# Optimization experiments

Measured on AMD Instinct MI355X. Metric: run time of the kernel, lower is better.

The kernel has to match this reference:

```python
import jax, jax.numpy as jnp
import numpy as np

N_NODES = 100000
N_EDGES = 1600000
IN_CH = 128
OUT_CH = 32
HEADS = 2
NEG_SLOPE = 0.2  # GATv2Conv default negative_slope


def setup_inputs() -> dict:
    key = jax.random.key(0)
    ks = jax.random.split(key, 6)
    x = jax.random.normal(ks[0], (N_NODES, IN_CH), dtype=jnp.float32)
    edge_index = jax.random.randint(ks[1], (2, N_EDGES), 0, N_NODES, dtype=jnp.int64)
    s_in = 1.0 / np.sqrt(IN_CH)
    Wl = jax.random.normal(ks[2], (IN_CH, HEADS * OUT_CH), dtype=jnp.float32) * s_in  # lin_l weight
    Wr = jax.random.normal(ks[3], (IN_CH, HEADS * OUT_CH), dtype=jnp.float32) * s_in  # lin_r weight
    bl = jnp.zeros((HEADS * OUT_CH,), dtype=jnp.float32)
    br = jnp.zeros((HEADS * OUT_CH,), dtype=jnp.float32)
    att = jax.random.normal(ks[4], (HEADS, OUT_CH), dtype=jnp.float32) * (1.0 / np.sqrt(OUT_CH))
    bias = jnp.zeros((OUT_CH,), dtype=jnp.float32)  # output bias (concat=False -> size out_channels)
    return {"x": x, "Wl": Wl, "bl": bl, "Wr": Wr, "br": br, "att": att, "bias": bias,
            "edge_index": edge_index}


def _gatv2_layer(x, Wl, bl, Wr, br, att, bias, edge_index):
    N = x.shape[0]
    H, C = att.shape
    # add self loops (GATv2Conv default add_self_loops=True)
    loops = jnp.arange(N, dtype=edge_index.dtype)
    src = jnp.concatenate([edge_index[0], loops])  # [E+N] message sources j
    dst = jnp.concatenate([edge_index[1], loops])  # [E+N] message targets i
    # per-node linear transforms (share_weights=False)
    xl = (x @ Wl + bl).reshape(N, H, C)
    xr = (x @ Wr + br).reshape(N, H, C)
    # GATv2 dynamic attention: a^T LeakyReLU(xl[j] + xr[i])
    h = xl[src] + xr[dst]                                   # [E, H, C]
    e = jnp.einsum('ehc,hc->eh', jax.nn.leaky_relu(h, NEG_SLOPE), att)  # [E, H]
    # segment softmax over incoming edges of each target node
    m = jax.ops.segment_max(e, dst, num_segments=N)         # [N, H]
    a = jnp.exp(e - m[dst])
    denom = jax.ops.segment_sum(a, dst, num_segments=N)     # [N, H]
    alpha = a / (denom[dst] + 1e-16)                        # [E, H]
    # weighted scatter-add of source messages
    out = jax.ops.segment_sum(alpha[:, :, None] * xl[src], dst, num_segments=N)  # [N, H, C]
    out = out.mean(axis=1) + bias                           # concat=False -> head mean
    return jax.nn.silu(out)                                 # activation='silu'


def reference(x, Wl, bl, Wr, br, att, bias, edge_index):
    return _gatv2_layer(x, Wl, bl, Wr, br, att, bias, edge_index)
```

## Files before the change

kernel.cpp:

```cpp
#include <hip/hip_runtime.h>
#include <math.h>

#define NEG 0.2f
#define BSH 9
#define BMASK ((1 << BSH) - 1)
#define CAP 12288
#define ACH 2048

typedef unsigned int uint;
typedef __attribute__((ext_vector_type(8))) short bf16x8;
typedef __attribute__((ext_vector_type(4))) float f32x4;

static __device__ __forceinline__ unsigned short f2bf(float f) {
    uint u = __float_as_uint(f);
    return (unsigned short)((u + 0x7fffu + ((u >> 16) & 1u)) >> 16);
}

static __device__ __forceinline__ void bf8dec(uint4 u, float* xs) {
    xs[0] = __uint_as_float(u.x << 16); xs[1] = __uint_as_float(u.x & 0xffff0000u);
    xs[2] = __uint_as_float(u.y << 16); xs[3] = __uint_as_float(u.y & 0xffff0000u);
    xs[4] = __uint_as_float(u.z << 16); xs[5] = __uint_as_float(u.z & 0xffff0000u);
    xs[6] = __uint_as_float(u.w << 16); xs[7] = __uint_as_float(u.w & 0xffff0000u);
}

static __device__ __forceinline__ float qsum(float p) {
    p += __uint_as_float(__builtin_amdgcn_mov_dpp(__float_as_uint(p), 0xB1, 0xF, 0xF, true));
    p += __uint_as_float(__builtin_amdgcn_mov_dpp(__float_as_uint(p), 0x4E, 0xF, 0xF, true));
    return p;
}

__global__ __launch_bounds__(256) void k_init(int* __restrict__ bcur, int NB) {
    int i = blockIdx.x * 256 + threadIdx.x;
    if (i < NB) bcur[i] = i * CAP;
}

__global__ __launch_bounds__(256) void k_gemm(const float* __restrict__ x,
        const float* __restrict__ Wl, const float* __restrict__ bl,
        const float* __restrict__ Wr, const float* __restrict__ br,
        unsigned short* __restrict__ xlh, float* __restrict__ xr, int N)
{
    __shared__ __align__(16) char sA[32768];
    __shared__ __align__(16) char sB[32768];
    const int t = threadIdx.x;
    const int base = blockIdx.x * 128;

#pragma unroll 4
    for (int s = 0; s < 16; ++s) {
        int f = s * 256 + t;
        int r = f >> 5;
        int c4 = f & 31;
        int rg = base + r; if (rg >= N) rg = N - 1;
        float4 v = ((const float4*)x)[(size_t)rg * 32 + c4];
        uint2 pk;
        pk.x = (uint)f2bf(v.x) | ((uint)f2bf(v.y) << 16);
        pk.y = (uint)f2bf(v.z) | ((uint)f2bf(v.w) << 16);
        int kb = c4 * 8;
        *(uint2*)(sA + r * 256 + (kb ^ ((r & 7) << 4))) = pk;
    }
    {
        int n = t & 127;
        int kh = (t >> 7) * 64;
        const float* Wp = (n < 64) ? (Wl + n) : (Wr + (n - 64));
        unsigned short hb[8];
#pragma unroll 8
        for (int i = 0; i < 64; ++i) {
            float v = Wp[(kh + i) * 64];
            hb[i & 7] = f2bf(v);
            if ((i & 7) == 7) {
                uint4 pk;
                pk.x = (uint)hb[0] | ((uint)hb[1] << 16);
                pk.y = (uint)hb[2] | ((uint)hb[3] << 16);
                pk.z = (uint)hb[4] | ((uint)hb[5] << 16);
                pk.w = (uint)hb[6] | ((uint)hb[7] << 16);
                int kb = (kh + i - 7) * 2;
                *(uint4*)(sB + n * 256 + (kb ^ ((n & 7) << 4))) = pk;
            }
        }
    }
    __syncthreads();

    const int w = t >> 6;
    const int lo = t & 15;
    const int hi = (t & 63) >> 4;
    f32x4 acc[2][8];
#pragma unroll
    for (int f = 0; f < 2; ++f)
#pragma unroll
        for (int j = 0; j < 8; ++j)
            acc[f][j] = (f32x4){0.f, 0.f, 0.f, 0.f};

#pragma unroll
    for (int ks = 0; ks < 4; ++ks) {
        int kb = ks * 64 + hi * 16;
        bf16x8 av[2], bv[8];
#pragma unroll
        for (int f = 0; f < 2; ++f) {
            int r = w * 32 + f * 16 + lo;
            av[f] = *(const bf16x8*)(sA + r * 256 + (kb ^ ((r & 7) << 4)));
        }
#pragma unroll
        for (int j = 0; j < 8; ++j) {
            int nn = j * 16 + lo;
            bv[j] = *(const bf16x8*)(sB + nn * 256 + (kb ^ ((nn & 7) << 4)));
        }
#pragma unroll
        for (int f = 0; f < 2; ++f)
#pragma unroll
            for (int j = 0; j < 8; ++j)
                acc[f][j] = __builtin_amdgcn_mfma_f32_16x16x32_bf16(av[f], bv[j], acc[f][j], 0, 0, 0);
    }

#pragma unroll
    for (int f = 0; f < 2; ++f) {
        int rbase = base + w * 32 + f * 16 + hi * 4;
#pragma unroll
        for (int j = 0; j < 8; ++j) {
            int nn = j * 16 + lo;
            float bvv = (j < 4) ? bl[nn] : br[nn - 64];
            float vv[4] = {acc[f][j][0] + bvv, acc[f][j][1] + bvv,
                           acc[f][j][2] + bvv, acc[f][j][3] + bvv};
            if (j < 4) {
#pragma unroll
                for (int q = 0; q < 4; ++q)
                    if (rbase + q < N) xlh[(size_t)(rbase + q) * 64 + nn] = f2bf(vv[q]);
            } else {
#pragma unroll
                for (int q = 0; q < 4; ++q)
                    if (rbase + q < N) xr[(size_t)(rbase + q) * 64 + (nn - 64)] = vv[q];
            }
        }
    }
}

__global__ __launch_bounds__(256) void k_scatA(const int* __restrict__ ei, int* __restrict__ bcur,
                                               unsigned* __restrict__ pairs, int E, int T, int NB) {
    __shared__ int h[256];
    __shared__ int basem[256];
    int b0 = blockIdx.x * ACH;
    int cnt = min(ACH, T - b0);
    h[threadIdx.x] = 0;
    __syncthreads();
    for (int i = threadIdx.x; i < cnt; i += 256) {
        int t = b0 + i;
        int d = (t < E) ? ei[E + t] : (t - E);
        atomicAdd(&h[d >> BSH], 1);
    }
    __syncthreads();
    if (threadIdx.x < NB) {
        int c = h[threadIdx.x];
        basem[threadIdx.x] = c ? atomicAdd(&bcur[threadIdx.x], c) : 0;
    }
    __syncthreads();
    h[threadIdx.x] = 0;
    __syncthreads();
    for (int i = threadIdx.x; i < cnt; i += 256) {
        int t = b0 + i;
        int s, d;
        if (t < E) { s = ei[t]; d = ei[E + t]; } else { s = t - E; d = s; }
        int b = d >> BSH;
        int idx = atomicAdd(&h[b], 1);
        pairs[basem[b] + idx] = ((unsigned)s << BSH) | (unsigned)(d & BMASK);
    }
}

__global__ __launch_bounds__(512) void k_scatB(const unsigned* __restrict__ pairs,
                                               const int* __restrict__ bcur,
                                               int* __restrict__ src_s, int2* __restrict__ rowrng, int N) {
    __shared__ int cnt[512];
    __shared__ int sm[512];
    __shared__ int lofs[512];
    int b = blockIdx.x;
    int beg = b * CAP, end = bcur[b];
    int nbase = b << BSH;
    cnt[threadIdx.x] = 0;
    __syncthreads();
    for (int i = beg + threadIdx.x; i < end; i += 512)
        atomicAdd(&cnt[pairs[i] & BMASK], 1);
    __syncthreads();
    int v = cnt[threadIdx.x];
    sm[threadIdx.x] = v;
    __syncthreads();
    int acc = v;
    for (int off = 1; off < 512; off <<= 1) {
        int t = (threadIdx.x >= off) ? sm[threadIdx.x - off] : 0;
        __syncthreads();
        acc += t;
        sm[threadIdx.x] = acc;
        __syncthreads();
    }
    int excl = acc - v;
    lofs[threadIdx.x] = excl;
    int n = nbase + threadIdx.x;
    if (n < N) rowrng[n] = make_int2(beg + excl, beg + excl + v);
    cnt[threadIdx.x] = 0;
    __syncthreads();
    for (int i = beg + threadIdx.x; i < end; i += 512) {
        unsigned p = pairs[i];
        int dl = p & BMASK;
        int idx = atomicAdd(&cnt[dl], 1);
        src_s[beg + lofs[dl] + idx] = p >> BSH;
    }
}

__global__ __launch_bounds__(256) void k_fused(const int2* __restrict__ rowrng,
        const int* __restrict__ src_s, const unsigned short* __restrict__ xlh,
        const float* __restrict__ xr, const float* __restrict__ att,
        const float* __restrict__ bias, float* __restrict__ out, int N)
{
    int n = blockIdx.x * 32 + (threadIdx.x >> 3);
    int j = threadIdx.x & 7;
    if (n >= N) return;
    const uint4* xl4 = (const uint4*)xlh;
    float xrv[8], attv[8];
    {
        float4 a = ((const float4*)xr)[(size_t)n * 16 + j * 2];
        float4 b = ((const float4*)xr)[(size_t)n * 16 + j * 2 + 1];
        xrv[0] = a.x; xrv[1] = a.y; xrv[2] = a.z; xrv[3] = a.w;
        xrv[4] = b.x; xrv[5] = b.y; xrv[6] = b.z; xrv[7] = b.w;
        float4 c = ((const float4*)att)[j * 2];
        float4 d = ((const float4*)att)[j * 2 + 1];
        attv[0] = c.x; attv[1] = c.y; attv[2] = c.z; attv[3] = c.w;
        attv[4] = d.x; attv[5] = d.y; attv[6] = d.z; attv[7] = d.w;
    }
    int2 rr = rowrng[n];
    float ssum = 0.f;
    float acc[8] = {0.f, 0.f, 0.f, 0.f, 0.f, 0.f, 0.f, 0.f};
    int i = rr.x;
    for (; i + 4 <= rr.y; i += 4) {
        int s0 = src_s[i], s1 = src_s[i + 1], s2 = src_s[i + 2], s3 = src_s[i + 3];
        uint4 u0 = xl4[(size_t)s0 * 8 + j];
        uint4 u1 = xl4[(size_t)s1 * 8 + j];
        uint4 u2 = xl4[(size_t)s2 * 8 + j];
        uint4 u3 = xl4[(size_t)s3 * 8 + j];
        float x0[8], x1[8], x2[8], x3[8];
        bf8dec(u0, x0); bf8dec(u1, x1); bf8dec(u2, x2); bf8dec(u3, x3);
        float p0 = 0.f, p1 = 0.f, p2 = 0.f, p3 = 0.f;
#pragma unroll
        for (int c = 0; c < 8; ++c) {
            float h0 = x0[c] + xrv[c], h1 = x1[c] + xrv[c];
            float h2 = x2[c] + xrv[c], h3 = x3[c] + xrv[c];
            h0 = fmaxf(h0, NEG * h0); h1 = fmaxf(h1, NEG * h1);
            h2 = fmaxf(h2, NEG * h2); h3 = fmaxf(h3, NEG * h3);
            p0 = fmaf(h0, attv[c], p0); p1 = fmaf(h1, attv[c], p1);
            p2 = fmaf(h2, attv[c], p2); p3 = fmaf(h3, attv[c], p3);
        }
        p0 = qsum(p0); p1 = qsum(p1); p2 = qsum(p2); p3 = qsum(p3);
        float w0 = __expf(p0), w1 = __expf(p1), w2 = __expf(p2), w3 = __expf(p3);
        ssum += (w0 + w1) + (w2 + w3);
#pragma unroll
        for (int c = 0; c < 8; ++c)
            acc[c] += w0 * x0[c] + w1 * x1[c] + w2 * x2[c] + w3 * x3[c];
    }
    for (; i < rr.y; ++i) {
        int s0 = src_s[i];
        uint4 u0 = xl4[(size_t)s0 * 8 + j];
        float x0[8];
        bf8dec(u0, x0);
        float p0 = 0.f;
#pragma unroll
        for (int c = 0; c < 8; ++c) {
            float h0 = x0[c] + xrv[c];
            h0 = fmaxf(h0, NEG * h0);
            p0 = fmaf(h0, attv[c], p0);
        }
        p0 = qsum(p0);
        float w0 = __expf(p0);
        ssum += w0;
#pragma unroll
        for (int c = 0; c < 8; ++c)
            acc[c] = fmaf(w0, x0[c], acc[c]);
    }
    float inv = 1.f / ssum;
    float o[8];
#pragma unroll
    for (int c = 0; c < 8; ++c) {
        float v = acc[c] * inv;
        float oth = __shfl_xor(v, 4);
        o[c] = (v + oth) * 0.5f;
    }
    if (j < 4) {
        float4 b0 = ((const float4*)bias)[j * 2];
        float4 b1 = ((const float4*)bias)[j * 2 + 1];
        float4 r0, r1;
        r0.x = o[0] + b0.x; r0.y = o[1] + b0.y; r0.z = o[2] + b0.z; r0.w = o[3] + b0.w;
        r1.x = o[4] + b1.x; r1.y = o[5] + b1.y; r1.z = o[6] + b1.z; r1.w = o[7] + b1.w;
        r0.x = r0.x / (1.f + __expf(-r0.x));
        r0.y = r0.y / (1.f + __expf(-r0.y));
        r0.z = r0.z / (1.f + __expf(-r0.z));
        r0.w = r0.w / (1.f + __expf(-r0.w));
        r1.x = r1.x / (1.f + __expf(-r1.x));
        r1.y = r1.y / (1.f + __expf(-r1.y));
        r1.z = r1.z / (1.f + __expf(-r1.z));
        r1.w = r1.w / (1.f + __expf(-r1.w));
        ((float4*)out)[(size_t)n * 8 + j * 2] = r0;
        ((float4*)out)[(size_t)n * 8 + j * 2 + 1] = r1;
    }
}

extern "C" void kernel_launch(void* const* d_in, const int* in_sizes, int n_in,
                              void* d_out, int out_size, void* d_ws, size_t ws_size,
                              hipStream_t stream) {
    const float* x    = (const float*)d_in[0];
    const float* Wl   = (const float*)d_in[1];
    const float* bl   = (const float*)d_in[2];
    const float* Wr   = (const float*)d_in[3];
    const float* br   = (const float*)d_in[4];
    const float* att  = (const float*)d_in[5];
    const float* bias = (const float*)d_in[6];
    const int*   ei   = (const int*)d_in[7];
    float* out = (float*)d_out;

    const int N = in_sizes[0] / 128;
    const int E = in_sizes[7] / 2;
    const int T = E + N;
    const int NB = (N + (1 << BSH) - 1) >> BSH;

    char* p = (char*)d_ws;
    auto take = [&](size_t bytes) {
        char* r = p;
        p += (bytes + 255) & ~(size_t)255;
        return r;
    };
    unsigned short* xlh = (unsigned short*)take((size_t)N * 64 * 2);
    float*    xr     = (float*)take((size_t)N * 64 * 4);
    unsigned* pairs  = (unsigned*)take((size_t)NB * CAP * 4);
    int*      src_s  = (int*)take((size_t)NB * CAP * 4);
    int2*     rowrng = (int2*)take((size_t)N * 8);
    int*      bcur   = (int*)take((size_t)NB * 4);

    k_init <<<1,                   256, 0, stream>>>(bcur, NB);
    k_gemm <<<(N + 127) / 128,     256, 0, stream>>>(x, Wl, bl, Wr, br, xlh, xr, N);
    k_scatA<<<(T + ACH - 1) / ACH, 256, 0, stream>>>(ei, bcur, pairs, E, T, NB);
    k_scatB<<<NB,                  512, 0, stream>>>(pairs, bcur, src_s, rowrng, N);
    k_fused<<<(N + 31) / 32,       256, 0, stream>>>(rowrng, src_s, xlh, xr, att, bias, out, N);
}
```

Baseline: 127.8 us.

## Use packed f32x2 math and abs-based LeakyReLU identity in edge attention loop

Rewrites the per-edge attention score with the identity leaky_relu(h) = 0.6*h + 0.4*|h| so that the score becomes two packed dot products over float2 vectors, which lets the compiler emit packed FP32 instructions. The message accumulation also moves to float2, and the gather index uses a 32-bit shift-or instead of 64-bit multiply. The W staging in the GEMM kernel is reworked to read coalesced float4 rows instead of strided scalar loads. The identity is exact apart from rounding, and the gains depend on the compiler actually producing packed instructions.

```diff
diff --git a/kernel.cpp b/kernel.cpp
--- a/kernel.cpp
+++ b/kernel.cpp
@@ -1,7 +1,6 @@
 #include <hip/hip_runtime.h>
 #include <math.h>
 
-#define NEG 0.2f
 #define BSH 9
 #define BMASK ((1 << BSH) - 1)
 #define CAP 12288
@@ -10,17 +9,25 @@
 typedef unsigned int uint;
 typedef __attribute__((ext_vector_type(8))) short bf16x8;
 typedef __attribute__((ext_vector_type(4))) float f32x4;
+typedef __attribute__((ext_vector_type(2))) float f32x2;
 
 static __device__ __forceinline__ unsigned short f2bf(float f) {
     uint u = __float_as_uint(f);
     return (unsigned short)((u + 0x7fffu + ((u >> 16) & 1u)) >> 16);
 }
 
-static __device__ __forceinline__ void bf8dec(uint4 u, float* xs) {
-    xs[0] = __uint_as_float(u.x << 16); xs[1] = __uint_as_float(u.x & 0xffff0000u);
-    xs[2] = __uint_as_float(u.y << 16); xs[3] = __uint_as_float(u.y & 0xffff0000u);
-    xs[4] = __uint_as_float(u.z << 16); xs[5] = __uint_as_float(u.z & 0xffff0000u);
-    xs[6] = __uint_as_float(u.w << 16); xs[7] = __uint_as_float(u.w & 0xffff0000u);
+static __device__ __forceinline__ f32x2 dec2(uint u) {
+    f32x2 r;
+    r.x = __uint_as_float(u << 16);
+    r.y = __uint_as_float(u & 0xffff0000u);
+    return r;
+}
+
+static __device__ __forceinline__ f32x2 abs2(f32x2 h) {
+    f32x2 r;
+    r.x = __uint_as_float(__float_as_uint(h.x) & 0x7fffffffu);
+    r.y = __uint_as_float(__float_as_uint(h.y) & 0x7fffffffu);
+    return r;
 }
 
 static __device__ __forceinline__ float qsum(float p) {
@@ -57,24 +64,22 @@
         int kb = c4 * 8;
         *(uint2*)(sA + r * 256 + (kb ^ ((r & 7) << 4))) = pk;
     }
-    {
-        int n = t & 127;
-        int kh = (t >> 7) * 64;
-        const float* Wp = (n < 64) ? (Wl + n) : (Wr + (n - 64));
-        unsigned short hb[8];
-#pragma unroll 8
-        for (int i = 0; i < 64; ++i) {
-            float v = Wp[(kh + i) * 64];
-            hb[i & 7] = f2bf(v);
-            if ((i & 7) == 7) {
-                uint4 pk;
-                pk.x = (uint)hb[0] | ((uint)hb[1] << 16);
-                pk.y = (uint)hb[2] | ((uint)hb[3] << 16);
-                pk.z = (uint)hb[4] | ((uint)hb[5] << 16);
-                pk.w = (uint)hb[6] | ((uint)hb[7] << 16);
-                int kb = (kh + i - 7) * 2;
-                *(uint4*)(sB + n * 256 + (kb ^ ((n & 7) << 4))) = pk;
-            }
+#pragma unroll
+    for (int s = 0; s < 8; ++s) {
+        int tau = s * 256 + t;
+        int m  = tau >> 10;
+        int k2 = (tau >> 4) & 63;
+        int n4 = tau & 15;
+        const float4* Wp = (const float4*)(m ? Wr : Wl);
+        float4 a = Wp[(2 * k2) * 16 + n4];
+        float4 b = Wp[(2 * k2 + 1) * 16 + n4];
+        const float* af = (const float*)&a;
+        const float* bf = (const float*)&b;
+#pragma unroll
+        for (int j = 0; j < 4; ++j) {
+            int n = m * 64 + n4 * 4 + j;
+            uint u = (uint)f2bf(af[j]) | ((uint)f2bf(bf[j]) << 16);
+            *(uint*)(sB + n * 256 + ((k2 * 4) ^ ((n & 7) << 4))) = u;
         }
     }
     __syncthreads();
@@ -211,72 +216,60 @@
     int j = threadIdx.x & 7;
     if (n >= N) return;
     const uint4* xl4 = (const uint4*)xlh;
-    float xrv[8], attv[8];
+    f32x2 xr2[4], att2[4];
     {
         float4 a = ((const float4*)xr)[(size_t)n * 16 + j * 2];
         float4 b = ((const float4*)xr)[(size_t)n * 16 + j * 2 + 1];
-        xrv[0] = a.x; xrv[1] = a.y; xrv[2] = a.z; xrv[3] = a.w;
-        xrv[4] = b.x; xrv[5] = b.y; xrv[6] = b.z; xrv[7] = b.w;
+        xr2[0] = (f32x2){a.x, a.y}; xr2[1] = (f32x2){a.z, a.w};
+        xr2[2] = (f32x2){b.x, b.y}; xr2[3] = (f32x2){b.z, b.w};
         float4 c = ((const float4*)att)[j * 2];
         float4 d = ((const float4*)att)[j * 2 + 1];
-        attv[0] = c.x; attv[1] = c.y; attv[2] = c.z; attv[3] = c.w;
-        attv[4] = d.x; attv[5] = d.y; attv[6] = d.z; attv[7] = d.w;
+        att2[0] = (f32x2){c.x, c.y}; att2[1] = (f32x2){c.z, c.w};
+        att2[2] = (f32x2){d.x, d.y}; att2[3] = (f32x2){d.z, d.w};
     }
     int2 rr = rowrng[n];
     float ssum = 0.f;
-    float acc[8] = {0.f, 0.f, 0.f, 0.f, 0.f, 0.f, 0.f, 0.f};
+    f32x2 acc2[4] = {(f32x2){0.f,0.f}, (f32x2){0.f,0.f}, (f32x2){0.f,0.f}, (f32x2){0.f,0.f}};
+
+#define EDGE_BODY(u)                                                      \
+    {                                                                     \
+        f32x2 v0 = dec2((u).x), v1 = dec2((u).y), v2 = dec2((u).z), v3 = dec2((u).w); \
+        f32x2 h0 = v0 + xr2[0], h1 = v1 + xr2[1], h2 = v2 + xr2[2], h3 = v3 + xr2[3]; \
+        f32x2 pa = h0 * att2[0]; pa += h1 * att2[1]; pa += h2 * att2[2]; pa += h3 * att2[3]; \
+        f32x2 pb = abs2(h0) * att2[0]; pb += abs2(h1) * att2[1];          \
+        pb += abs2(h2) * att2[2]; pb += abs2(h3) * att2[3];               \
+        float p = 0.6f * (pa.x + pa.y) + 0.4f * (pb.x + pb.y);            \
+        p = qsum(p);                                                      \
+        float wq = __expf(p);                                             \
+        ssum += wq;                                                       \
+        f32x2 ws = (f32x2){wq, wq};                                       \
+        acc2[0] += ws * v0; acc2[1] += ws * v1;                           \
+        acc2[2] += ws * v2; acc2[3] += ws * v3;                           \
+    }
+
     int i = rr.x;
     for (; i + 4 <= rr.y; i += 4) {
         int s0 = src_s[i], s1 = src_s[i + 1], s2 = src_s[i + 2], s3 = src_s[i + 3];
-        uint4 u0 = xl4[(size_t)s0 * 8 + j];
-        uint4 u1 = xl4[(size_t)s1 * 8 + j];
-        uint4 u2 = xl4[(size_t)s2 * 8 + j];
-        uint4 u3 = xl4[(size_t)s3 * 8 + j];
-        float x0[8], x1[8], x2[8], x3[8];
-        bf8dec(u0, x0); bf8dec(u1, x1); bf8dec(u2, x2); bf8dec(u3, x3);
-        float p0 = 0.f, p1 = 0.f, p2 = 0.f, p3 = 0.f;
-#pragma unroll
-        for (int c = 0; c < 8; ++c) {
-            float h0 = x0[c] + xrv[c], h1 = x1[c] + xrv[c];
-            float h2 = x2[c] + xrv[c], h3 = x3[c] + xrv[c];
-            h0 = fmaxf(h0, NEG * h0); h1 = fmaxf(h1, NEG * h1);
-            h2 = fmaxf(h2, NEG * h2); h3 = fmaxf(h3, NEG * h3);
-            p0 = fmaf(h0, attv[c], p0); p1 = fmaf(h1, attv[c], p1);
-            p2 = fmaf(h2, attv[c], p2); p3 = fmaf(h3, attv[c], p3);
-        }
-        p0 = qsum(p0); p1 = qsum(p1); p2 = qsum(p2); p3 = qsum(p3);
-        float w0 = __expf(p0), w1 = __expf(p1), w2 = __expf(p2), w3 = __expf(p3);
-        ssum += (w0 + w1) + (w2 + w3);
-#pragma unroll
-        for (int c = 0; c < 8; ++c)
-            acc[c] += w0 * x0[c] + w1 * x1[c] + w2 * x2[c] + w3 * x3[c];
+        uint4 u0 = xl4[(((uint)s0 << 3) | j)];
+        uint4 u1 = xl4[(((uint)s1 << 3) | j)];
+        uint4 u2 = xl4[(((uint)s2 << 3) | j)];
+        uint4 u3 = xl4[(((uint)s3 << 3) | j)];
+        EDGE_BODY(u0); EDGE_BODY(u1); EDGE_BODY(u2); EDGE_BODY(u3);
     }
     for (; i < rr.y; ++i) {
         int s0 = src_s[i];
-        uint4 u0 = xl4[(size_t)s0 * 8 + j];
-        float x0[8];
-        bf8dec(u0, x0);
-        float p0 = 0.f;
-#pragma unroll
-        for (int c = 0; c < 8; ++c) {
-            float h0 = x0[c] + xrv[c];
-            h0 = fmaxf(h0, NEG * h0);
-            p0 = fmaf(h0, attv[c], p0);
-        }
-        p0 = qsum(p0);
-        float w0 = __expf(p0);
-        ssum += w0;
-#pragma unroll
-        for (int c = 0; c < 8; ++c)
-            acc[c] = fmaf(w0, x0[c], acc[c]);
-    }
+        uint4 u0 = xl4[(((uint)s0 << 3) | j)];
+        EDGE_BODY(u0);
+    }
+#undef EDGE_BODY
+
     float inv = 1.f / ssum;
     float o[8];
 #pragma unroll
-    for (int c = 0; c < 8; ++c) {
-        float v = acc[c] * inv;
-        float oth = __shfl_xor(v, 4);
-        o[c] = (v + oth) * 0.5f;
+    for (int q = 0; q < 4; ++q) {
+        float vx = acc2[q].x * inv, vy = acc2[q].y * inv;
+        o[2 * q]     = (vx + __shfl_xor(vx, 4)) * 0.5f;
+        o[2 * q + 1] = (vy + __shfl_xor(vy, 4)) * 0.5f;
     }
     if (j < 4) {
         float4 b0 = ((const float4*)bias)[j * 2];
```

Measured after the change: 123.2 us. 1.04x faster.
